# Optimization experiments

Hardware: AMD Instinct MI355X
Metric: run time of the kernel (lower is better)

## Reference

```python
import jax, jax.numpy as jnp
import numpy as np

B, N, C = 64, 197, 768
H = 12
L, KAPPA = 4, 16


def setup_inputs() -> dict:
    key = jax.random.key(0)
    ks = jax.random.split(key, 7)
    src = jax.random.normal(ks[0], (B, N, C), jnp.float32)
    vtm_memory = jax.random.normal(ks[1], (L, B, KAPPA, C), jnp.float32)
    Wq = jax.random.normal(ks[2], (C, C), jnp.float32) * 0.02
    Wk = jax.random.normal(ks[3], (C, C), jnp.float32) * 0.02
    Wv = jax.random.normal(ks[4], (C, C), jnp.float32) * 0.02
    Wp = jax.random.normal(ks[5], (C, C), jnp.float32) * 0.02
    bp = jnp.zeros((C,), jnp.float32)
    return {"src": src, "vtm_memory": vtm_memory, "Wq": Wq, "Wk": Wk, "Wv": Wv, "Wp": Wp, "bp": bp}


def reference(src, vtm_memory, Wq, Wk, Wv, Wp, bp):
    Bb, Nn, Cc = src.shape
    hd = Cc // H
    scale = hd ** -0.5
    Ll, _, Tt, _ = vtm_memory.shape
    # stack per-layer memories -> [B, L*kappa, C], concat with src as KV
    vtm_tokens = vtm_memory.transpose(1, 0, 2, 3).reshape(Bb, Ll * Tt, Cc)
    kv = jnp.concatenate([src, vtm_tokens], axis=1)  # [B, N+L*kappa, C]
    Nkv = kv.shape[1]
    # VTM_ATTN cross-attention (bias-free qkv, biased proj; dropout = identity)
    q = (src @ Wq.T).reshape(Bb, Nn, H, hd).transpose(0, 2, 1, 3)    # [B,H,N,hd]
    k = (kv @ Wk.T).reshape(Bb, Nkv, H, hd).transpose(0, 2, 1, 3)    # [B,H,Nkv,hd]
    v = (kv @ Wv.T).reshape(Bb, Nkv, H, hd).transpose(0, 2, 1, 3)
    attn = jax.nn.softmax(jnp.einsum('bhqd,bhkd->bhqk', q, k) * scale, axis=-1)
    attn_out = attn[:, :, :, :Nn]  # self-part slice, detached in original
    x = jnp.einsum('bhqk,bhkd->bhqd', attn, v).transpose(0, 2, 1, 3).reshape(Bb, Nn, Cc)
    x = x @ Wp.T + bp
    # register_memory: CLS-row saliency over non-CLS keys, topk gather from src
    saliency = attn_out.mean(axis=1)[:, 0, 1:]          # [B, N-1]
    _, top_idx = jax.lax.top_k(saliency, KAPPA)          # [B, kappa]
    salient_tokens = jnp.take_along_axis(src, top_idx[:, :, None], axis=1)  # [B, kappa, C]
    return (x, attn_out, salient_tokens)
```

## Files before the change

### kernel.cpp

```cpp
#include <hip/hip_runtime.h>
#include <cstdint>

typedef _Float16 half8 __attribute__((ext_vector_type(8)));
typedef float f32x4 __attribute__((ext_vector_type(4)));
typedef unsigned short u16;

typedef __attribute__((address_space(3))) char lds_char;
typedef const __attribute__((address_space(1))) char glb_char;
#define GLOAD16(gp, lp) \
  __builtin_amdgcn_global_load_lds((glb_char*)(gp), (lds_char*)(lp), 16, 0, 0)

#define B_ 64
#define NQ 197
#define C_ 768
#define H_ 12
#define NKV 261
#define RKV 16768
#define RQ  12672

#define X_OFF    0
#define ATTN_OFF 9682944
#define SAL_OFF  39488256

#define WS_WQKV  0u
#define WS_WP    3538944u
#define WS_KV    4718592u
#define WS_QKV   30474240u
#define WS_O     107741184u
#define WS_Q0    (WS_KV + 0u)
#define WS_P     (WS_KV + 196608u)
#define WS_R     (WS_KV + 1048576u)

__device__ __forceinline__ u16 f2h(float f) {
  return __builtin_bit_cast(u16, (_Float16)f);
}

__global__ void wconv(const float* __restrict__ Wq, const float* __restrict__ Wk,
                      const float* __restrict__ Wv, const float* __restrict__ Wp,
                      u16* __restrict__ Wqkv, u16* __restrict__ Wph) {
  for (int i = blockIdx.x * blockDim.x + threadIdx.x; i < 4 * 147456;
       i += gridDim.x * blockDim.x) {
    int g = i / 147456;
    int idx = (i - g * 147456) * 4;
    const float* s = (g == 0) ? Wq : (g == 1) ? Wk : (g == 2) ? Wv : Wp;
    float4 v = *(const float4*)(s + idx);
    union { u16 u[4]; uint64_t q; } o;
    o.u[0] = f2h(v.x); o.u[1] = f2h(v.y); o.u[2] = f2h(v.z); o.u[3] = f2h(v.w);
    u16* d = (g < 3) ? (Wqkv + (size_t)g * 589824 + idx) : (Wph + idx);
    *(uint64_t*)d = o.q;
  }
}

__global__ void build_kv(const float* __restrict__ src, const float* __restrict__ vtm,
                         u16* __restrict__ kvh) {
  const int total = RKV * 192;
  for (int i = blockIdx.x * blockDim.x + threadIdx.x; i < total;
       i += gridDim.x * blockDim.x) {
    int row = i / 192;
    int c = (i - row * 192) * 4;
    union { u16 u[4]; uint64_t q; } o;
    if (row < B_ * NKV) {
      int b = row / NKV, t = row - b * NKV;
      const float* p;
      if (t < NQ) p = src + ((size_t)b * NQ + t) * 768 + c;
      else {
        int tt = t - NQ;
        p = vtm + ((size_t)((tt >> 4) * 64 + b) * 16 + (tt & 15)) * 768 + c;
      }
      float4 v = *(const float4*)p;
      o.u[0] = f2h(v.x); o.u[1] = f2h(v.y); o.u[2] = f2h(v.z); o.u[3] = f2h(v.w);
    } else {
      o.q = 0;
    }
    *(uint64_t*)(kvh + (size_t)row * 768 + c) = o.q;
  }
}

template <int EPI>
__launch_bounds__(256, 4)
__global__ void gemm_bt(const u16* __restrict__ A, const u16* __restrict__ Bw,
                        void* __restrict__ Cp, const float* __restrict__ bias,
                        int ntiles, int kdim, int lda, int ldb, int ldc, int mlimit) {
  __shared__ u16 sA[128 * 64];
  __shared__ u16 sB[128 * 64];
  const int tid = threadIdx.x;
  const int w = tid >> 6, lane = tid & 63;
  int bid = blockIdx.x;
  {
    const int nwg = gridDim.x;
    const int q = nwg >> 3, rr = nwg & 7;
    const int xcd = bid & 7, loc = bid >> 3;
    bid = (xcd < rr ? xcd * (q + 1) : rr * (q + 1) + (xcd - rr) * q) + loc;
  }
  const int nt = bid % ntiles, mt = bid / ntiles;
  const int wr = w >> 1, wc = w & 1;
  const int fr = lane & 15, g = lane >> 4;
  const int frs = fr & 7;

  const u16* gAp[4];
  const u16* gBp[4];
#pragma unroll
  for (int j = 0; j < 4; ++j) {
    const int lin = j * 256 + tid;
    const int r = lin >> 3;
    const int c = (lin & 7) ^ (r & 7);
    gAp[j] = A + (size_t)(mt * 128 + r) * lda + c * 8;
    gBp[j] = Bw + (size_t)(nt * 128 + r) * ldb + c * 8;
  }

  const f32x4 vz = {0.f, 0.f, 0.f, 0.f};
  f32x4 acc[4][4];
#pragma unroll
  for (int i = 0; i < 4; ++i)
#pragma unroll
    for (int j = 0; j < 4; ++j) acc[i][j] = vz;

  for (int k0 = 0; k0 < kdim; k0 += 64) {
    __syncthreads();
#pragma unroll
    for (int j = 0; j < 4; ++j)
      GLOAD16(gAp[j] + k0, ((char*)sA) + (j * 256 + tid) * 16);
#pragma unroll
    for (int j = 0; j < 4; ++j)
      GLOAD16(gBp[j] + k0, ((char*)sB) + (j * 256 + tid) * 16);
    __syncthreads();
#pragma unroll
    for (int kk = 0; kk < 2; ++kk) {
      half8 af[4], bf[4];
      const int sw = ((kk * 4 + g) ^ frs) * 8;
#pragma unroll
      for (int i = 0; i < 4; ++i) {
        af[i] = *(const half8*)&sA[(wr * 64 + i * 16 + fr) * 64 + sw];
        bf[i] = *(const half8*)&sB[(wc * 64 + i * 16 + fr) * 64 + sw];
      }
#pragma unroll
      for (int mi = 0; mi < 4; ++mi)
#pragma unroll
        for (int ni = 0; ni < 4; ++ni)
          acc[mi][ni] =
              __builtin_amdgcn_mfma_f32_16x16x32_f16(af[mi], bf[ni], acc[mi][ni], 0, 0, 0);
    }
  }

  const int rbase = (lane >> 4) << 2;
#pragma unroll
  for (int mi = 0; mi < 4; ++mi) {
#pragma unroll
    for (int ni = 0; ni < 4; ++ni) {
      const int n = nt * 128 + wc * 64 + ni * 16 + fr;
#pragma unroll
      for (int r = 0; r < 4; ++r) {
        const int m = mt * 128 + wr * 64 + mi * 16 + rbase + r;
        if (EPI == 0) {
          ((u16*)Cp)[(size_t)m * ldc + n] = f2h(acc[mi][ni][r]);
        } else {
          if (m < mlimit) ((float*)Cp)[(size_t)m * ldc + n] = acc[mi][ni][r] + bias[n];
        }
      }
    }
  }
}

#define ATT_LDS_TOT 79872

__launch_bounds__(256, 2)
__global__ void attn_kernel(const u16* __restrict__ qkv, float* __restrict__ out,
                            u16* __restrict__ Oh) {
  extern __shared__ char smem[];
  const int tid = threadIdx.x, w = tid >> 6, lane = tid & 63;
  const int bid = blockIdx.x;
  const int b = bid / 12, h = bid - b * 12;
  const size_t rowbase = (size_t)b * NKV;

  for (int i = tid; i < 272 * 8; i += 256) {
    const int row = i >> 3, c8 = (i & 7) << 3;
    uint4 v = *(const uint4*)(qkv + (rowbase + row) * 2304 + 768 + h * 64 + c8);
    *(uint4*)(smem + row * 128 + ((c8 * 2) ^ ((row & 7) << 4))) = v;
  }
  for (int i = tid; i < 288 * 8; i += 256) {
    const int row = i >> 3, c8 = (i & 7) << 3;
    union { u16 u[8]; uint4 v; } t;
    t.v = *(const uint4*)(qkv + (rowbase + row) * 2304 + 1536 + h * 64 + c8);
#pragma unroll
    for (int j = 0; j < 8; ++j) {
      const int d = c8 + j;
      const int sw = ((row < 256) ? (d & 7) : (d & 3)) << 4;
      *(u16*)(smem + 34816 + d * 576 + ((row * 2) ^ sw)) = t.u[j];
    }
  }
  __syncthreads();

  const int fr = lane & 15, g = lane >> 4;
  char* PcBase = smem + 71680 + (w << 11);
  const f32x4 vz = {0.f, 0.f, 0.f, 0.f};

  for (int qt = w; qt < 13; qt += 4) {
    const u16* qp = qkv + (rowbase + qt * 16 + fr) * 2304 + h * 64 + g * 8;
    half8 aq0 = *(const half8*)qp;
    half8 aq1 = *(const half8*)(qp + 32);

    f32x4 sc[17];
#pragma unroll
    for (int jt = 0; jt < 17; ++jt) {
      const int krow = jt * 16 + fr;
      const int swz = (krow & 7) << 4;
      half8 bk0 = *(const half8*)(smem + krow * 128 + ((g * 16) ^ swz));
      half8 bk1 = *(const half8*)(smem + krow * 128 + ((64 + g * 16) ^ swz));
      f32x4 a = vz;
      a = __builtin_amdgcn_mfma_f32_16x16x32_f16(aq0, bk0, a, 0, 0, 0);
      a = __builtin_amdgcn_mfma_f32_16x16x32_f16(aq1, bk1, a, 0, 0, 0);
      sc[jt] = a;
    }
#pragma unroll
    for (int jt = 0; jt < 17; ++jt) {
      const bool valid = (jt * 16 + fr) < NKV;
#pragma unroll
      for (int ri = 0; ri < 4; ++ri)
        sc[jt][ri] = valid ? sc[jt][ri] * 0.125f : -3.0e38f;
    }
#pragma unroll
    for (int ri = 0; ri < 4; ++ri) {
      float m = sc[0][ri];
#pragma unroll
      for (int jt = 1; jt < 17; ++jt) m = fmaxf(m, sc[jt][ri]);
#pragma unroll
      for (int off = 1; off <= 8; off <<= 1) m = fmaxf(m, __shfl_xor(m, off, 64));
      float s = 0.f;
#pragma unroll
      for (int jt = 0; jt < 17; ++jt) {
        float e = __expf(sc[jt][ri] - m);
        sc[jt][ri] = e;
        s += e;
      }
#pragma unroll
      for (int off = 1; off <= 8; off <<= 1) s += __shfl_xor(s, off, 64);
      const float inv = 1.f / s;
#pragma unroll
      for (int jt = 0; jt < 17; ++jt) sc[jt][ri] *= inv;
    }
    const int q0r = qt * 16 + g * 4;
    {
      float* ob = out + ATTN_OFF + (size_t)bid * NQ * NQ;
#pragma unroll
      for (int jt = 0; jt < 13; ++jt) {
        const int col = jt * 16 + fr;
        if (col < NQ) {
#pragma unroll
          for (int ri = 0; ri < 4; ++ri) {
            const int qr = q0r + ri;
            if (qr < NQ) ob[(size_t)qr * NQ + col] = sc[jt][ri];
          }
        }
      }
    }
    f32x4 oa[4] = {vz, vz, vz, vz};
#pragma unroll
    for (int kt = 0; kt < 9; ++kt) {
      char* pcb = PcBase + (kt & 1) * 1024;
#pragma unroll
      for (int hf = 0; hf < 2; ++hf) {
        const int jt = kt * 2 + hf;
#pragma unroll
        for (int ri = 0; ri < 4; ++ri) {
          const int prow = g * 4 + ri, pcol = hf * 16 + fr;
          const float v = (jt < 17) ? sc[jt][ri] : 0.f;
          *(u16*)(pcb + prow * 64 + ((pcol * 2) ^ ((prow & 3) << 4))) = f2h(v);
        }
      }
      asm volatile("s_waitcnt lgkmcnt(0)" ::: "memory");
      __builtin_amdgcn_sched_barrier(0);
      half8 pa = *(const half8*)(pcb + fr * 64 + ((g * 16) ^ ((fr & 3) << 4)));
#pragma unroll
      for (int dt = 0; dt < 4; ++dt) {
        const int vrow = dt * 16 + fr;
        const int sw = ((kt < 8) ? (vrow & 7) : (vrow & 3)) << 4;
        half8 bv = *(const half8*)(smem + 34816 + vrow * 576 + ((kt * 64 + g * 16) ^ sw));
        oa[dt] = __builtin_amdgcn_mfma_f32_16x16x32_f16(pa, bv, oa[dt], 0, 0, 0);
      }
    }
#pragma unroll
    for (int dt = 0; dt < 4; ++dt)
#pragma unroll
      for (int ri = 0; ri < 4; ++ri) {
        const int qr = q0r + ri;
        if (qr < NQ)
          Oh[((size_t)b * NQ + qr) * 768 + h * 64 + dt * 16 + fr] = f2h(oa[dt][ri]);
      }
  }
}

__global__ void sal_q0(const float* __restrict__ src, const float* __restrict__ Wq,
                       float* __restrict__ q0ws) {
  const int bid = blockIdx.x;
  const int b = bid / 192, cb = (bid - (bid / 192) * 192) * 4;
  const int w = threadIdx.x >> 6, lane = threadIdx.x & 63;
  const int c = cb + w;
  const float* srow = src + (size_t)b * NQ * 768;
  const float* wrow = Wq + (size_t)c * 768;
  float acc = 0.f;
#pragma unroll
  for (int j = 0; j < 12; ++j)
    acc = fmaf(srow[lane + 64 * j], wrow[lane + 64 * j], acc);
#pragma unroll
  for (int off = 32; off >= 1; off >>= 1) acc += __shfl_xor(acc, off, 64);
  if (lane == 0) q0ws[(size_t)b * 768 + c] = acc;
}

__global__ void sal_r(const float* __restrict__ q0ws, const float* __restrict__ Wk,
                      float* __restrict__ rws) {
  const int bid = blockIdx.x;
  const int b = bid / 36, rem = bid - (bid / 36) * 36;
  const int h = rem / 3, cc = (rem - (rem / 3) * 3) * 256;
  const int c = cc + threadIdx.x;
  __shared__ float sq[64];
  if (threadIdx.x < 64) sq[threadIdx.x] = q0ws[(size_t)b * 768 + h * 64 + threadIdx.x];
  __syncthreads();
  float acc = 0.f;
#pragma unroll
  for (int dh = 0; dh < 64; ++dh)
    acc = fmaf(sq[dh], Wk[(size_t)(h * 64 + dh) * 768 + c], acc);
  rws[((size_t)b * 12 + h) * 768 + c] = acc;
}

__global__ void sal_p(const float* __restrict__ src, const float* __restrict__ vtm,
                      const float* __restrict__ rws, float* __restrict__ pws) {
  const int bid = blockIdx.x;
  const int b = bid / NKV, kk = bid - (bid / NKV) * NKV;
  const int w = threadIdx.x >> 6, lane = threadIdx.x & 63;
  const float* kvrow;
  if (kk < NQ) kvrow = src + ((size_t)b * NQ + kk) * 768;
  else {
    int tt = kk - NQ;
    kvrow = vtm + ((size_t)((tt >> 4) * 64 + b) * 16 + (tt & 15)) * 768;
  }
  float v[12];
#pragma unroll
  for (int j = 0; j < 12; ++j) v[j] = kvrow[lane + 64 * j];
  for (int hh = w; hh < 12; hh += 4) {
    const float* rrow = rws + ((size_t)b * 12 + hh) * 768;
    float acc = 0.f;
#pragma unroll
    for (int j = 0; j < 12; ++j) acc = fmaf(v[j], rrow[lane + 64 * j], acc);
#pragma unroll
    for (int off = 32; off >= 1; off >>= 1) acc += __shfl_xor(acc, off, 64);
    if (lane == 0) pws[((size_t)b * 12 + hh) * NKV + kk] = acc * 0.125f;
  }
}

__global__ void sal_top(const float* __restrict__ src, const float* __restrict__ pws,
                        float* __restrict__ out) {
  const int b = blockIdx.x, tid = threadIdx.x, w = tid >> 6, lane = tid & 63;
  __shared__ float s_p[12][272];
  __shared__ float s_sal[196];
  __shared__ int s_top[16];
  for (int i = tid; i < 12 * NKV; i += 256)
    s_p[i / NKV][i - (i / NKV) * NKV] = pws[(size_t)b * 12 * NKV + i];
  __syncthreads();
  for (int hh = w; hh < 12; hh += 4) {
    float m = -3.0e38f;
    for (int kk = lane; kk < NKV; kk += 64) m = fmaxf(m, s_p[hh][kk]);
#pragma unroll
    for (int off = 32; off >= 1; off >>= 1) m = fmaxf(m, __shfl_xor(m, off, 64));
    float s = 0.f;
    for (int kk = lane; kk < NKV; kk += 64) s += expf(s_p[hh][kk] - m);
#pragma unroll
    for (int off = 32; off >= 1; off >>= 1) s += __shfl_xor(s, off, 64);
    for (int kk = lane; kk < NKV; kk += 64) s_p[hh][kk] = expf(s_p[hh][kk] - m) / s;
  }
  __syncthreads();
  if (tid < 196) {
    float a = 0.f;
#pragma unroll
    for (int hh = 0; hh < 12; ++hh) a += s_p[hh][tid + 1];
    s_sal[tid] = a * (1.0f / 12.0f);
  }
  __syncthreads();
  if (w == 0) {
    float v[4];
    int idx[4];
    bool taken[4];
#pragma unroll
    for (int j = 0; j < 4; ++j) {
      int id = lane + 64 * j;
      idx[j] = id;
      taken[j] = false;
      v[j] = (id < 196) ? s_sal[id] : -3.0e38f;
    }
    for (int round = 0; round < 16; ++round) {
      float best = -3.0e38f;
      int bi = 1 << 30;
#pragma unroll
      for (int j = 0; j < 4; ++j)
        if (!taken[j] && v[j] > best) { best = v[j]; bi = idx[j]; }
#pragma unroll
      for (int off = 1; off <= 32; off <<= 1) {
        float ov = __shfl_xor(best, off, 64);
        int oi = __shfl_xor(bi, off, 64);
        if (ov > best || (ov == best && oi < bi)) { best = ov; bi = oi; }
      }
#pragma unroll
      for (int j = 0; j < 4; ++j)
        if (idx[j] == bi) taken[j] = true;
      if (lane == 0) s_top[round] = bi;
    }
  }
  __syncthreads();
  for (int i = 0; i < 16; ++i) {
    int id = s_top[i];
    for (int c = tid; c < 768; c += 256)
      out[SAL_OFF + ((size_t)b * 16 + i) * 768 + c] = src[((size_t)b * NQ + id) * 768 + c];
  }
}

extern "C" void kernel_launch(void* const* d_in, const int* in_sizes, int n_in,
                              void* d_out, int out_size, void* d_ws, size_t ws_size,
                              hipStream_t stream) {
  const float* src = (const float*)d_in[0];
  const float* vtm = (const float*)d_in[1];
  const float* Wq = (const float*)d_in[2];
  const float* Wk = (const float*)d_in[3];
  const float* Wv = (const float*)d_in[4];
  const float* Wp = (const float*)d_in[5];
  const float* bp = (const float*)d_in[6];
  float* out = (float*)d_out;
  char* ws = (char*)d_ws;

  u16* Wqkv = (u16*)(ws + WS_WQKV);
  u16* Wph = (u16*)(ws + WS_WP);
  u16* kvh = (u16*)(ws + WS_KV);
  u16* QKV = (u16*)(ws + WS_QKV);
  u16* Oh = (u16*)(ws + WS_O);
  float* q0ws = (float*)(ws + WS_Q0);
  float* pws = (float*)(ws + WS_P);
  float* rws = (float*)(ws + WS_R);

  wconv<<<1152, 256, 0, stream>>>(Wq, Wk, Wv, Wp, Wqkv, Wph);
  build_kv<<<2048, 256, 0, stream>>>(src, vtm, kvh);
  gemm_bt<0><<<131 * 18, 256, 0, stream>>>(kvh, Wqkv, QKV, nullptr, 18, 768, 768, 768, 2304, 0);
  hipFuncSetAttribute((const void*)attn_kernel, hipFuncAttributeMaxDynamicSharedMemorySize,
                      ATT_LDS_TOT);
  attn_kernel<<<B_ * H_, 256, ATT_LDS_TOT, stream>>>(QKV, out, Oh);
  gemm_bt<1><<<99 * 6, 256, 0, stream>>>(Oh, Wph, out, bp, 6, 768, 768, 768, 768, 12608);
  sal_q0<<<64 * 192, 256, 0, stream>>>(src, Wq, q0ws);
  sal_r<<<64 * 12 * 3, 256, 0, stream>>>(q0ws, Wk, rws);
  sal_p<<<64 * NKV, 256, 0, stream>>>(src, vtm, rws, pws);
  sal_top<<<64, 256, 0, stream>>>(src, pws, out);
}
```

Baseline: 297.8 us.

## Stage fp16 GEMM epilogue through LDS and fold softmax scale into Q

The fp16 GEMM epilogue now writes the accumulator tile into swizzled LDS and then emits 16-byte coalesced global stores, replacing the scattered 2-byte stores. The attention kernel pre-scales Q by 0.125 in fp16, which is exact since it is a power of two, and masks only the last key tile instead of scaling every score. It also drops the explicit lgkmcnt wait and sched_barrier between the P write to LDS and its read. That read is a cross-lane exchange within a wave, so correctness now relies on the compiler inserting the wait itself.

```diff
diff --git a/kernel.cpp b/kernel.cpp
--- a/kernel.cpp
+++ b/kernel.cpp
@@ -81,8 +81,9 @@
 __global__ void gemm_bt(const u16* __restrict__ A, const u16* __restrict__ Bw,
                         void* __restrict__ Cp, const float* __restrict__ bias,
                         int ntiles, int kdim, int lda, int ldb, int ldc, int mlimit) {
-  __shared__ u16 sA[128 * 64];
-  __shared__ u16 sB[128 * 64];
+  __shared__ u16 sAB[2][128 * 64];
+  u16* sA = sAB[0];
+  u16* sB = sAB[1];
   const int tid = threadIdx.x;
   const int w = tid >> 6, lane = tid & 63;
   int bid = blockIdx.x;
@@ -142,18 +143,43 @@
     }
   }
 
-  const int rbase = (lane >> 4) << 2;
-#pragma unroll
-  for (int mi = 0; mi < 4; ++mi) {
-#pragma unroll
-    for (int ni = 0; ni < 4; ++ni) {
-      const int n = nt * 128 + wc * 64 + ni * 16 + fr;
-#pragma unroll
-      for (int r = 0; r < 4; ++r) {
-        const int m = mt * 128 + wr * 64 + mi * 16 + rbase + r;
-        if (EPI == 0) {
-          ((u16*)Cp)[(size_t)m * ldc + n] = f2h(acc[mi][ni][r]);
-        } else {
+  if (EPI == 0) {
+    u16* tile = sAB[0];
+    __syncthreads();
+#pragma unroll
+    for (int mi = 0; mi < 4; ++mi)
+#pragma unroll
+      for (int ni = 0; ni < 4; ++ni) {
+        const int n = wc * 64 + ni * 16 + fr;
+#pragma unroll
+        for (int r = 0; r < 4; ++r) {
+          const int m = wr * 64 + mi * 16 + (g << 2) + r;
+          tile[m * 128 + (n ^ ((m & 7) << 3))] = f2h(acc[mi][ni][r]);
+        }
+      }
+    __syncthreads();
+    const int r8 = lane >> 3, ck = lane & 7;
+#pragma unroll
+    for (int s = 0; s < 4; ++s) {
+      const int row = w * 32 + s * 8 + r8;
+      const int gm = mt * 128 + row;
+#pragma unroll
+      for (int hc = 0; hc < 2; ++hc) {
+        const int nb = hc * 64 + ck * 8;
+        uint4 v = *(const uint4*)&tile[row * 128 + (nb ^ ((row & 7) << 3))];
+        *(uint4*)&((u16*)Cp)[(size_t)gm * ldc + nt * 128 + nb] = v;
+      }
+    }
+  } else {
+    const int rbase = (lane >> 4) << 2;
+#pragma unroll
+    for (int mi = 0; mi < 4; ++mi) {
+#pragma unroll
+      for (int ni = 0; ni < 4; ++ni) {
+        const int n = nt * 128 + wc * 64 + ni * 16 + fr;
+#pragma unroll
+        for (int r = 0; r < 4; ++r) {
+          const int m = mt * 128 + wr * 64 + mi * 16 + rbase + r;
           if (m < mlimit) ((float*)Cp)[(size_t)m * ldc + n] = acc[mi][ni][r] + bias[n];
         }
       }
@@ -198,6 +224,8 @@
     const u16* qp = qkv + (rowbase + qt * 16 + fr) * 2304 + h * 64 + g * 8;
     half8 aq0 = *(const half8*)qp;
     half8 aq1 = *(const half8*)(qp + 32);
+    aq0 = aq0 * (_Float16)0.125;
+    aq1 = aq1 * (_Float16)0.125;
 
     f32x4 sc[17];
 #pragma unroll
@@ -211,12 +239,9 @@
       a = __builtin_amdgcn_mfma_f32_16x16x32_f16(aq1, bk1, a, 0, 0, 0);
       sc[jt] = a;
     }
-#pragma unroll
-    for (int jt = 0; jt < 17; ++jt) {
-      const bool valid = (jt * 16 + fr) < NKV;
-#pragma unroll
-      for (int ri = 0; ri < 4; ++ri)
-        sc[jt][ri] = valid ? sc[jt][ri] * 0.125f : -3.0e38f;
+    if (fr >= 5) {
+#pragma unroll
+      for (int ri = 0; ri < 4; ++ri) sc[16][ri] = -3.0e38f;
     }
 #pragma unroll
     for (int ri = 0; ri < 4; ++ri) {
@@ -267,8 +292,6 @@
           *(u16*)(pcb + prow * 64 + ((pcol * 2) ^ ((prow & 3) << 4))) = f2h(v);
         }
       }
-      asm volatile("s_waitcnt lgkmcnt(0)" ::: "memory");
-      __builtin_amdgcn_sched_barrier(0);
       half8 pa = *(const half8*)(pcb + fr * 64 + ((g * 16) ^ ((fr & 3) << 4)));
 #pragma unroll
       for (int dt = 0; dt < 4; ++dt) {
```

New measurement: 295.9 us. Within noise of the previous version (-0.6%).
